# Kernel tuning notes

Measured on AMD Instinct MI355X. Metric: run time of the kernel, lower is better.

The kernel has to match this reference:

```python
import jax, jax.numpy as jnp
import numpy as np

DIM = 384
NH = 12
HEAD = DIM // NH
WS = (7, 7, 7)
L = WS[0] * WS[1] * WS[2]          # 343 tokens per window
NW = 64                             # number of windows (mask.shape[0])
B = 1                               # batch per window group
N = B * NW                          # leading dim of x
TBL = (2 * WS[0] - 1) * (2 * WS[1] - 1) * (2 * WS[2] - 1)  # 2197
SCALE = HEAD ** -0.5


def _rel_index():
    # Standard Swin 3D relative position index, shape (L, L), values in [0, TBL)
    coords = np.stack(np.meshgrid(*[np.arange(w) for w in WS], indexing='ij')).reshape(3, -1)  # (3, L)
    rel = coords[:, :, None] - coords[:, None, :]                     # (3, L, L)
    rel = rel + (np.array(WS) - 1)[:, None, None]                     # shift to >= 0
    s1 = (2 * WS[1] - 1) * (2 * WS[2] - 1)
    s2 = (2 * WS[2] - 1)
    idx = rel[0] * s1 + rel[1] * s2 + rel[2]
    return jnp.asarray(idx, jnp.int32)


def setup_inputs() -> dict:
    key = jax.random.key(0)
    k_x, k_m, k_qkv, k_tbl, k_pw = jax.random.split(key, 5)
    x = jax.random.normal(k_x, (N, L, DIM), dtype=jnp.float32)
    mask = jax.random.bernoulli(k_m, 0.5, (NW, L, L))                 # bool, True = masked
    qkv_w = jax.random.normal(k_qkv, (DIM, 3 * DIM), dtype=jnp.float32) * 0.02
    table = jax.random.normal(k_tbl, (TBL, NH), dtype=jnp.float32) * 0.02
    proj_w = jax.random.normal(k_pw, (DIM, DIM), dtype=jnp.float32) * 0.02
    proj_b = jnp.zeros((DIM,), dtype=jnp.float32)
    rel_idx = _rel_index()
    return {"x": x, "qkv_w": qkv_w, "table": table, "proj_w": proj_w,
            "proj_b": proj_b, "mask": mask, "rel_idx": rel_idx}


def reference(x, qkv_w, table, proj_w, proj_b, mask, rel_idx):
    n, l, _ = x.shape
    # QKV projection (no bias, qkv_bias=False)
    qkv = (x @ qkv_w).reshape(n, l, 3, NH, HEAD).transpose(2, 0, 3, 1, 4)  # (3, n, nh, l, ch)
    q, k, v = qkv[0], qkv[1], qkv[2]
    attn = jnp.einsum('nhlc,nhmc->nhlm', q * SCALE, k)                 # (n, nh, l, l)
    # gather relative position bias: (L*L, nh) -> (nh, L, L)
    bias = table[rel_idx.reshape(-1)].reshape(l, l, NH).transpose(2, 0, 1)
    attn = attn + bias[None]
    # per-window boolean mask: attn viewed as (batch, nw, nh, l, l)
    attn = attn.reshape(-1, NW, NH, l, l)
    attn = jnp.where(mask[None, :, None], -jnp.inf, attn).reshape(n, NH, l, l)
    attn = jax.nn.softmax(attn, axis=-1)
    out = jnp.einsum('nhlm,nhmc->nhlc', attn, v)                       # (n, nh, l, ch)
    out = out.transpose(0, 2, 1, 3).reshape(n, l, DIM)
    return out @ proj_w + proj_b
```

## Files before the change

### kernel.cpp

```cpp
#include <hip/hip_runtime.h>


#define DIMD 384
#define NHH 12
#define HEADD 32
#define LL 343
#define NWW 64
#define NTOK (NWW * LL)
#define MPT 176
#define MP (MPT * 128)
#define LP 352
#define QT 22
#define KS 40
#define VTS 360
#define PSB 40
#define MW 12
#define SCALE_ 0.17677669529663687f
#define LOG2E_ 1.4426950408889634f
#define NEGBIG_ (-1.0e4f)

typedef _Float16 f16;
typedef _Float16 v8h __attribute__((ext_vector_type(8)));
typedef _Float16 v4h __attribute__((ext_vector_type(4)));
typedef float v4f __attribute__((ext_vector_type(4)));

__device__ __forceinline__ void async_cp16(const void* g, void* l) {
    __builtin_amdgcn_global_load_lds(
        (const __attribute__((address_space(1))) void*)g,
        (__attribute__((address_space(3))) void*)l, 16, 0, 0);
}

constexpr size_t QKV_ELEMS = (size_t)NWW * NHH * LL * HEADD;
constexpr size_t OFF_Q    = 0;
constexpr size_t OFF_K    = OFF_Q  + QKV_ELEMS * 2;
constexpr size_t OFF_V    = OFF_K  + QKV_ELEMS * 2;
constexpr size_t OFF_AO   = OFF_V  + QKV_ELEMS * 2;
constexpr size_t OFF_BT   = OFF_AO + (size_t)MP * DIMD * 2;
constexpr size_t OFF_WT   = OFF_BT + (size_t)NHH * LP * LP * 4;
constexpr size_t OFF_PWT  = OFF_WT + (size_t)3 * DIMD * DIMD * 2;
constexpr size_t OFF_MTB  = OFF_PWT + (size_t)DIMD * DIMD * 2;

constexpr int SMEM_ATTN = LP * KS * 2 + 32 * VTS * 2 + LP * MW * 4 + 8 * 16 * PSB * 2;

#define S0 (NTOK * DIMD / 4)
#define S1 (3 * DIMD * DIMD)
#define S2 (DIMD * DIMD)
#define S3 (NHH * LP * LP)
#define S4 (NWW * MW * LP)
#define SPREP (S0 + S1 + S2 + S3 + S4)

__global__ __launch_bounds__(256) void prep_all(
    const float* __restrict__ x, f16* __restrict__ xh,
    const float* __restrict__ qkv_w, f16* __restrict__ wt,
    const float* __restrict__ proj_w, f16* __restrict__ pwt,
    const float* __restrict__ table, const int* __restrict__ rel, float* __restrict__ btf,
    const int* __restrict__ mask, unsigned int* __restrict__ mtb) {
    int t = blockIdx.x * 256 + threadIdx.x;
    if (t < S0) {
        float4 v = *(const float4*)(x + (size_t)t * 4);
        v4h o; o[0] = (f16)v.x; o[1] = (f16)v.y; o[2] = (f16)v.z; o[3] = (f16)v.w;
        *(v4h*)(xh + (size_t)t * 4) = o;
    } else if (t < S0 + S1) {
        int e = t - S0;
        int n = e / DIMD, k = e % DIMD;
        wt[e] = (f16)qkv_w[(size_t)k * (3 * DIMD) + n];
    } else if (t < S0 + S1 + S2) {
        int e = t - S0 - S1;
        int n = e / DIMD, k = e % DIMD;
        pwt[e] = (f16)proj_w[(size_t)k * DIMD + n];
    } else if (t < S0 + S1 + S2 + S3) {
        int e = t - S0 - S1 - S2;
        int h = e / (LP * LP), rem = e % (LP * LP);
        int rq = rem / (LP * 4);
        int rem2 = rem % (LP * 4);
        int col = rem2 >> 2, e2 = rem2 & 3;
        int r = rq * 4 + e2;
        float v = NEGBIG_;
        if (col < LL && r < LL) v = table[(size_t)rel[r * LL + col] * NHH + h] * LOG2E_;
        btf[e] = v;
    } else if (t < SPREP) {
        int e = t - S0 - S1 - S2 - S3;
        int n = e / (MW * LP), rem = e % (MW * LP);
        int wg = rem / LP, col = rem % LP;
        unsigned int wd = 0;
        if (col < LL) {
            int rbase = wg * 32;
#pragma unroll 4
            for (int b = 0; b < 32; ++b) {
                int r = rbase + b;
                if (r < LL && mask[((size_t)n * LL + r) * LL + col]) wd |= (1u << b);
            }
        }
        mtb[((size_t)n * LP + col) * MW + wg] = wd;
    }
}

__global__ __launch_bounds__(256) void qkv_gemm(
    const f16* __restrict__ xh, const f16* __restrict__ wt,
    f16* __restrict__ qb, f16* __restrict__ kb, f16* __restrict__ vb) {
    __shared__ f16 As[128 * 32];
    __shared__ f16 Bs[128 * 32];
    const int lin = blockIdx.x;
    const int m0 = ((lin / 72) * 8 + (lin & 7)) * 128;
    const int n0 = ((lin >> 3) % 9) * 128;
    const int tid = threadIdx.x;
    const int wave = tid >> 6, lane = tid & 63;
    const int quad = lane >> 4, l15 = lane & 15;
    const int wm = (wave >> 1) * 64, wn = (wave & 1) * 64;
    const int srow = (lane >> 2);
    const int scol = (lane & 3) * 8;
    const f16* ga0 = xh + (size_t)(m0 + wave * 32 + srow) * DIMD + scol;
    const f16* ga1 = xh + (size_t)(m0 + wave * 32 + 16 + srow) * DIMD + scol;
    const f16* gb0 = wt + (size_t)(n0 + wave * 32 + srow) * DIMD + scol;
    const f16* gb1 = wt + (size_t)(n0 + wave * 32 + 16 + srow) * DIMD + scol;
    f16* la0 = As + (wave * 2) * 512;
    f16* la1 = As + (wave * 2 + 1) * 512;
    f16* lb0 = Bs + (wave * 2) * 512;
    f16* lb1 = Bs + (wave * 2 + 1) * 512;
    v4f acc[4][4] = {};
    for (int k0 = 0; k0 < DIMD; k0 += 32) {
        async_cp16(ga0 + k0, la0);
        async_cp16(ga1 + k0, la1);
        async_cp16(gb0 + k0, lb0);
        async_cp16(gb1 + k0, lb1);
        __syncthreads();
        v8h a[4], b[4];
#pragma unroll
        for (int i = 0; i < 4; ++i) a[i] = *(const v8h*)(As + (wm + i * 16 + l15) * 32 + quad * 8);
#pragma unroll
        for (int j = 0; j < 4; ++j) b[j] = *(const v8h*)(Bs + (wn + j * 16 + l15) * 32 + quad * 8);
#pragma unroll
        for (int i = 0; i < 4; ++i)
#pragma unroll
            for (int j = 0; j < 4; ++j)
                acc[i][j] = __builtin_amdgcn_mfma_f32_16x16x32_f16(a[i], b[j], acc[i][j], 0, 0, 0);
        __syncthreads();
    }
#pragma unroll
    for (int i = 0; i < 4; ++i)
#pragma unroll
        for (int e = 0; e < 4; ++e) {
            int gm = m0 + wm + i * 16 + quad * 4 + e;
            if (gm < NTOK) {
                int win = gm / LL, tok = gm % LL;
#pragma unroll
                for (int j = 0; j < 4; ++j) {
                    int gn = n0 + wn + j * 16 + l15;
                    int t = gn / DIMD, rem = gn % DIMD;
                    int h = rem >> 5, ch = rem & 31;
                    f16* dst = (t == 0) ? qb : (t == 1) ? kb : vb;
                    float ov = acc[i][j][e];
                    if (t == 0) ov *= (SCALE_ * LOG2E_);
                    dst[(((size_t)(win * NHH + h)) * LL + tok) * HEADD + ch] = (f16)ov;
                }
            }
        }
}

__global__ __launch_bounds__(512, 4) void attn_kernel(
    const f16* __restrict__ qb, const f16* __restrict__ kb, const f16* __restrict__ vb,
    const float* __restrict__ biasT, const unsigned int* __restrict__ mtb,
    f16* __restrict__ ao) {
    extern __shared__ char smem[];
    f16* Ks  = (f16*)smem;
    f16* Vts = Ks + LP * KS;
    unsigned int* mtbL = (unsigned int*)(Vts + 32 * VTS);
    f16* Ps  = (f16*)(mtbL + LP * MW);
    const int n = blockIdx.x, h = blockIdx.y;
    const int tid = threadIdx.x, wave = tid >> 6, lane = tid & 63;
    const int quad = lane >> 4, l15 = lane & 15;
    const size_t slice = ((size_t)(n * NHH + h)) * (LL * HEADD);
    const f16* qg = qb + slice;
    const f16* kg = kb + slice;
    const f16* vg = vb + slice;
    for (int i = tid; i < LL * 8; i += 512) {
        int row = i >> 3, c4 = i & 7;
        *(ushort4*)(Ks + row * KS + c4 * 4) = *(const ushort4*)(kg + i * 4);
    }
    for (int i = tid; i < (LP - LL) * 8; i += 512) {
        int row = LL + (i >> 3), c4 = i & 7;
        *(ushort4*)(Ks + row * KS + c4 * 4) = make_ushort4(0, 0, 0, 0);
    }
    for (int i = tid; i < LL * 8; i += 512) {
        int key = i >> 3, c4 = (i & 7) * 4;
        ushort4 vv = *(const ushort4*)(vg + key * HEADD + c4);
        f16* d = Vts + c4 * VTS + key;
        d[0] = *(const f16*)&vv.x; d[VTS] = *(const f16*)&vv.y;
        d[2 * VTS] = *(const f16*)&vv.z; d[3 * VTS] = *(const f16*)&vv.w;
    }
    for (int i = tid; i < 32 * (LP - LL); i += 512) {
        int ch = i / (LP - LL), key = LL + i % (LP - LL);
        Vts[ch * VTS + key] = (f16)0.f;
    }
    {
        const unsigned int* mg = mtb + (size_t)n * LP * MW;
        for (int i = tid; i < LP * MW; i += 512) mtbL[i] = mg[i];
    }
    __syncthreads();
    f16* Pw = Ps + wave * (16 * PSB);
    const float* bth = biasT + (size_t)h * LP * LP;
    for (int qt = wave; qt < QT; qt += 8) {
        v8h af = *(const v8h*)(qg + (qt * 16 + l15) * HEADD + quad * 8);
        const int r0 = qt * 16 + quad * 4;
        const int rword = r0 >> 5, rsh = r0 & 31;
        const float* bq = bth + (size_t)(qt * 4 + quad) * (LP * 4);
        v4f rsum = {};
        v4f o0 = {}, o1 = {};
#pragma unroll
        for (int ktp = 0; ktp < 11; ++ktp) {
            v4f cin[2]; unsigned int mw[2]; v8h bf[2]; v4f s[2];
#pragma unroll
            for (int half = 0; half < 2; ++half) {
                const int col = (ktp * 2 + half) * 16 + l15;
                cin[half] = *(const v4f*)(bq + (size_t)col * 4);
                mw[half] = mtbL[col * MW + rword];
                bf[half] = *(const v8h*)(Ks + col * KS + quad * 8);
            }
#pragma unroll
            for (int half = 0; half < 2; ++half) {
                v4f c = cin[half];
#pragma unroll
                for (int e = 0; e < 4; ++e)
                    if ((mw[half] >> (rsh + e)) & 1u) c[e] = NEGBIG_;
                s[half] = __builtin_amdgcn_mfma_f32_16x16x32_f16(af, bf[half], c, 0, 0, 0);
            }
#pragma unroll
            for (int half = 0; half < 2; ++half)
#pragma unroll
                for (int e = 0; e < 4; ++e) {
                    float p = __builtin_amdgcn_exp2f(s[half][e]);
                    rsum[e] += p;
                    Pw[(quad * 4 + e) * PSB + half * 16 + l15] = (f16)p;
                }
            v8h a  = *(const v8h*)(Pw + l15 * PSB + quad * 8);
            v8h b0 = *(const v8h*)(Vts + l15 * VTS + ktp * 32 + quad * 8);
            v8h b1 = *(const v8h*)(Vts + (16 + l15) * VTS + ktp * 32 + quad * 8);
            o0 = __builtin_amdgcn_mfma_f32_16x16x32_f16(a, b0, o0, 0, 0, 0);
            o1 = __builtin_amdgcn_mfma_f32_16x16x32_f16(a, b1, o1, 0, 0, 0);
        }
#pragma unroll
        for (int e = 0; e < 4; ++e) {
            float t = rsum[e];
            t += __shfl_xor(t, 1);
            t += __shfl_xor(t, 2);
            t += __shfl_xor(t, 4);
            t += __shfl_xor(t, 8);
            rsum[e] = t;
        }
#pragma unroll
        for (int e = 0; e < 4; ++e) {
            int r = r0 + e;
            if (r < LL) {
                float inv = 1.f / rsum[e];
                f16* orow = ao + ((size_t)(n * LL + r)) * DIMD + h * HEADD;
                orow[l15] = (f16)(o0[e] * inv);
                orow[16 + l15] = (f16)(o1[e] * inv);
            }
        }
    }
}

__global__ __launch_bounds__(256) void proj_gemm(
    const f16* __restrict__ ao, const f16* __restrict__ pwt,
    const float* __restrict__ pb, float* __restrict__ out) {
    __shared__ f16 As[128 * 32];
    __shared__ f16 Bs[128 * 32];
    const int lin = blockIdx.x;
    const int m0 = ((lin / 24) * 8 + (lin & 7)) * 128;
    const int n0 = ((lin >> 3) % 3) * 128;
    const int tid = threadIdx.x;
    const int wave = tid >> 6, lane = tid & 63;
    const int quad = lane >> 4, l15 = lane & 15;
    const int wm = (wave >> 1) * 64, wn = (wave & 1) * 64;
    const int srow = (lane >> 2);
    const int scol = (lane & 3) * 8;
    const f16* ga0 = ao + (size_t)(m0 + wave * 32 + srow) * DIMD + scol;
    const f16* ga1 = ao + (size_t)(m0 + wave * 32 + 16 + srow) * DIMD + scol;
    const f16* gb0 = pwt + (size_t)(n0 + wave * 32 + srow) * DIMD + scol;
    const f16* gb1 = pwt + (size_t)(n0 + wave * 32 + 16 + srow) * DIMD + scol;
    f16* la0 = As + (wave * 2) * 512;
    f16* la1 = As + (wave * 2 + 1) * 512;
    f16* lb0 = Bs + (wave * 2) * 512;
    f16* lb1 = Bs + (wave * 2 + 1) * 512;
    v4f acc[4][4] = {};
    for (int k0 = 0; k0 < DIMD; k0 += 32) {
        async_cp16(ga0 + k0, la0);
        async_cp16(ga1 + k0, la1);
        async_cp16(gb0 + k0, lb0);
        async_cp16(gb1 + k0, lb1);
        __syncthreads();
        v8h a[4], b[4];
#pragma unroll
        for (int i = 0; i < 4; ++i) a[i] = *(const v8h*)(As + (wm + i * 16 + l15) * 32 + quad * 8);
#pragma unroll
        for (int j = 0; j < 4; ++j) b[j] = *(const v8h*)(Bs + (wn + j * 16 + l15) * 32 + quad * 8);
#pragma unroll
        for (int i = 0; i < 4; ++i)
#pragma unroll
            for (int j = 0; j < 4; ++j)
                acc[i][j] = __builtin_amdgcn_mfma_f32_16x16x32_f16(a[i], b[j], acc[i][j], 0, 0, 0);
        __syncthreads();
    }
#pragma unroll
    for (int i = 0; i < 4; ++i)
#pragma unroll
        for (int e = 0; e < 4; ++e) {
            int gm = m0 + wm + i * 16 + quad * 4 + e;
            if (gm < NTOK) {
#pragma unroll
                for (int j = 0; j < 4; ++j) {
                    int gn = n0 + wn + j * 16 + l15;
                    out[(size_t)gm * DIMD + gn] = acc[i][j][e] + pb[gn];
                }
            }
        }
}

extern "C" void kernel_launch(void* const* d_in, const int* in_sizes, int n_in,
                              void* d_out, int out_size, void* d_ws, size_t ws_size,
                              hipStream_t stream) {
    const float* x      = (const float*)d_in[0];
    const float* qkv_w  = (const float*)d_in[1];
    const float* table  = (const float*)d_in[2];
    const float* proj_w = (const float*)d_in[3];
    const float* proj_b = (const float*)d_in[4];
    const int* mask     = (const int*)d_in[5];
    const int* rel      = (const int*)d_in[6];
    float* out = (float*)d_out;
    char* ws = (char*)d_ws;

    f16* q    = (f16*)(ws + OFF_Q);
    f16* k    = (f16*)(ws + OFF_K);
    f16* v    = (f16*)(ws + OFF_V);
    f16* xh   = (f16*)(ws + OFF_AO);
    f16* ao   = (f16*)(ws + OFF_AO);
    float* bt = (float*)(ws + OFF_BT);
    f16* wt   = (f16*)(ws + OFF_WT);
    f16* pwt  = (f16*)(ws + OFF_PWT);
    unsigned int* mtb = (unsigned int*)(ws + OFF_MTB);

    hipFuncSetAttribute((const void*)attn_kernel,
                        hipFuncAttributeMaxDynamicSharedMemorySize, SMEM_ATTN);

    prep_all<<<(SPREP + 255) / 256, 256, 0, stream>>>(
        x, xh, qkv_w, wt, proj_w, pwt, table, rel, bt, mask, mtb);
    qkv_gemm<<<dim3(MPT * 9), 256, 0, stream>>>(xh, wt, q, k, v);
    attn_kernel<<<dim3(NWW, NHH), 512, SMEM_ATTN, stream>>>(q, k, v, bt, mtb, ao);
    proj_gemm<<<dim3(MPT * 3), 256, 0, stream>>>(ao, pwt, proj_b, out);
}
```

Before: 237.9 us.

## Fuse x fp32-to-fp16 conversion into QKV GEMM and use head-major QKV layout

Drops the separate x-to-fp16 conversion pass from the prep kernel. The QKV GEMM now loads fp32 x directly, converts it in registers and writes it to LDS, which saves one full write and read of the fp16 copy of x. The Q/K/V buffers change to a [head][token][ch] layout so the epilogue can use precomputed per-column offsets instead of per-element div/mod. The trade-off is that A-tile loads become synchronous fp32 loads rather than async LDS copies, and each x tile is re-read and re-converted by all 9 N-tiles.

```diff
diff --git a/kernel.cpp b/kernel.cpp
--- a/kernel.cpp
+++ b/kernel.cpp
@@ -30,11 +30,11 @@
         (__attribute__((address_space(3))) void*)l, 16, 0, 0);
 }
 
-constexpr size_t QKV_ELEMS = (size_t)NWW * NHH * LL * HEADD;
+constexpr size_t HBUF = (size_t)NHH * MP * HEADD * 2;
 constexpr size_t OFF_Q    = 0;
-constexpr size_t OFF_K    = OFF_Q  + QKV_ELEMS * 2;
-constexpr size_t OFF_V    = OFF_K  + QKV_ELEMS * 2;
-constexpr size_t OFF_AO   = OFF_V  + QKV_ELEMS * 2;
+constexpr size_t OFF_K    = OFF_Q  + HBUF;
+constexpr size_t OFF_V    = OFF_K  + HBUF;
+constexpr size_t OFF_AO   = OFF_V  + HBUF;
 constexpr size_t OFF_BT   = OFF_AO + (size_t)MP * DIMD * 2;
 constexpr size_t OFF_WT   = OFF_BT + (size_t)NHH * LP * LP * 4;
 constexpr size_t OFF_PWT  = OFF_WT + (size_t)3 * DIMD * DIMD * 2;
@@ -42,34 +42,28 @@
 
 constexpr int SMEM_ATTN = LP * KS * 2 + 32 * VTS * 2 + LP * MW * 4 + 8 * 16 * PSB * 2;
 
-#define S0 (NTOK * DIMD / 4)
 #define S1 (3 * DIMD * DIMD)
 #define S2 (DIMD * DIMD)
 #define S3 (NHH * LP * LP)
 #define S4 (NWW * MW * LP)
-#define SPREP (S0 + S1 + S2 + S3 + S4)
+#define SPREP (S1 + S2 + S3 + S4)
 
 __global__ __launch_bounds__(256) void prep_all(
-    const float* __restrict__ x, f16* __restrict__ xh,
     const float* __restrict__ qkv_w, f16* __restrict__ wt,
     const float* __restrict__ proj_w, f16* __restrict__ pwt,
     const float* __restrict__ table, const int* __restrict__ rel, float* __restrict__ btf,
     const int* __restrict__ mask, unsigned int* __restrict__ mtb) {
     int t = blockIdx.x * 256 + threadIdx.x;
-    if (t < S0) {
-        float4 v = *(const float4*)(x + (size_t)t * 4);
-        v4h o; o[0] = (f16)v.x; o[1] = (f16)v.y; o[2] = (f16)v.z; o[3] = (f16)v.w;
-        *(v4h*)(xh + (size_t)t * 4) = o;
-    } else if (t < S0 + S1) {
-        int e = t - S0;
+    if (t < S1) {
+        int e = t;
         int n = e / DIMD, k = e % DIMD;
         wt[e] = (f16)qkv_w[(size_t)k * (3 * DIMD) + n];
-    } else if (t < S0 + S1 + S2) {
-        int e = t - S0 - S1;
+    } else if (t < S1 + S2) {
+        int e = t - S1;
         int n = e / DIMD, k = e % DIMD;
         pwt[e] = (f16)proj_w[(size_t)k * DIMD + n];
-    } else if (t < S0 + S1 + S2 + S3) {
-        int e = t - S0 - S1 - S2;
+    } else if (t < S1 + S2 + S3) {
+        int e = t - S1 - S2;
         int h = e / (LP * LP), rem = e % (LP * LP);
         int rq = rem / (LP * 4);
         int rem2 = rem % (LP * 4);
@@ -79,7 +73,7 @@
         if (col < LL && r < LL) v = table[(size_t)rel[r * LL + col] * NHH + h] * LOG2E_;
         btf[e] = v;
     } else if (t < SPREP) {
-        int e = t - S0 - S1 - S2 - S3;
+        int e = t - S1 - S2 - S3;
         int n = e / (MW * LP), rem = e % (MW * LP);
         int wg = rem / LP, col = rem % LP;
         unsigned int wd = 0;
@@ -96,7 +90,7 @@
 }
 
 __global__ __launch_bounds__(256) void qkv_gemm(
-    const f16* __restrict__ xh, const f16* __restrict__ wt,
+    const float* __restrict__ x, const f16* __restrict__ wt,
     f16* __restrict__ qb, f16* __restrict__ kb, f16* __restrict__ vb) {
     __shared__ f16 As[128 * 32];
     __shared__ f16 Bs[128 * 32];
@@ -109,20 +103,29 @@
     const int wm = (wave >> 1) * 64, wn = (wave & 1) * 64;
     const int srow = (lane >> 2);
     const int scol = (lane & 3) * 8;
-    const f16* ga0 = xh + (size_t)(m0 + wave * 32 + srow) * DIMD + scol;
-    const f16* ga1 = xh + (size_t)(m0 + wave * 32 + 16 + srow) * DIMD + scol;
     const f16* gb0 = wt + (size_t)(n0 + wave * 32 + srow) * DIMD + scol;
     const f16* gb1 = wt + (size_t)(n0 + wave * 32 + 16 + srow) * DIMD + scol;
-    f16* la0 = As + (wave * 2) * 512;
-    f16* la1 = As + (wave * 2 + 1) * 512;
     f16* lb0 = Bs + (wave * 2) * 512;
     f16* lb1 = Bs + (wave * 2 + 1) * 512;
+    int arow[4]; const float* asrc[4];
+#pragma unroll
+    for (int i = 0; i < 4; ++i) {
+        int c = i * 256 + tid;
+        arow[i] = c >> 3;
+        int srcr = m0 + arow[i]; if (srcr >= NTOK) srcr = NTOK - 1;
+        asrc[i] = x + (size_t)srcr * DIMD + (c & 7) * 4;
+    }
     v4f acc[4][4] = {};
     for (int k0 = 0; k0 < DIMD; k0 += 32) {
-        async_cp16(ga0 + k0, la0);
-        async_cp16(ga1 + k0, la1);
         async_cp16(gb0 + k0, lb0);
         async_cp16(gb1 + k0, lb1);
+#pragma unroll
+        for (int i = 0; i < 4; ++i) {
+            int c = i * 256 + tid;
+            float4 v = *(const float4*)(asrc[i] + k0);
+            v4h o; o[0] = (f16)v.x; o[1] = (f16)v.y; o[2] = (f16)v.z; o[3] = (f16)v.w;
+            *(v4h*)(As + arow[i] * 32 + (c & 7) * 4) = o;
+        }
         __syncthreads();
         v8h a[4], b[4];
 #pragma unroll
@@ -136,23 +139,25 @@
                 acc[i][j] = __builtin_amdgcn_mfma_f32_16x16x32_f16(a[i], b[j], acc[i][j], 0, 0, 0);
         __syncthreads();
     }
+    const int t = n0 / DIMD;
+    f16* dst = (t == 0) ? qb : (t == 1) ? kb : vb;
+    const float sc = (t == 0) ? (SCALE_ * LOG2E_) : 1.0f;
+    size_t hoff[4];
+#pragma unroll
+    for (int j = 0; j < 4; ++j) {
+        int rem = (n0 - t * DIMD) + wn + j * 16 + l15;
+        hoff[j] = (size_t)(rem >> 5) * ((size_t)MP * HEADD) + (rem & 31);
+    }
 #pragma unroll
     for (int i = 0; i < 4; ++i)
 #pragma unroll
         for (int e = 0; e < 4; ++e) {
             int gm = m0 + wm + i * 16 + quad * 4 + e;
             if (gm < NTOK) {
-                int win = gm / LL, tok = gm % LL;
-#pragma unroll
-                for (int j = 0; j < 4; ++j) {
-                    int gn = n0 + wn + j * 16 + l15;
-                    int t = gn / DIMD, rem = gn % DIMD;
-                    int h = rem >> 5, ch = rem & 31;
-                    f16* dst = (t == 0) ? qb : (t == 1) ? kb : vb;
-                    float ov = acc[i][j][e];
-                    if (t == 0) ov *= (SCALE_ * LOG2E_);
-                    dst[(((size_t)(win * NHH + h)) * LL + tok) * HEADD + ch] = (f16)ov;
-                }
+                size_t g32 = (size_t)gm * HEADD;
+#pragma unroll
+                for (int j = 0; j < 4; ++j)
+                    dst[hoff[j] + g32] = (f16)(acc[i][j][e] * sc);
             }
         }
 }
@@ -169,7 +174,7 @@
     const int n = blockIdx.x, h = blockIdx.y;
     const int tid = threadIdx.x, wave = tid >> 6, lane = tid & 63;
     const int quad = lane >> 4, l15 = lane & 15;
-    const size_t slice = ((size_t)(n * NHH + h)) * (LL * HEADD);
+    const size_t slice = ((size_t)h * MP + n * LL) * HEADD;
     const f16* qg = qb + slice;
     const f16* kg = kb + slice;
     const f16* vg = vb + slice;
@@ -332,7 +337,6 @@
     f16* q    = (f16*)(ws + OFF_Q);
     f16* k    = (f16*)(ws + OFF_K);
     f16* v    = (f16*)(ws + OFF_V);
-    f16* xh   = (f16*)(ws + OFF_AO);
     f16* ao   = (f16*)(ws + OFF_AO);
     float* bt = (float*)(ws + OFF_BT);
     f16* wt   = (f16*)(ws + OFF_WT);
@@ -343,8 +347,8 @@
                         hipFuncAttributeMaxDynamicSharedMemorySize, SMEM_ATTN);
 
     prep_all<<<(SPREP + 255) / 256, 256, 0, stream>>>(
-        x, xh, qkv_w, wt, proj_w, pwt, table, rel, bt, mask, mtb);
-    qkv_gemm<<<dim3(MPT * 9), 256, 0, stream>>>(xh, wt, q, k, v);
+        qkv_w, wt, proj_w, pwt, table, rel, bt, mask, mtb);
+    qkv_gemm<<<dim3(MPT * 9), 256, 0, stream>>>(x, wt, q, k, v);
     attn_kernel<<<dim3(NWW, NHH), 512, SMEM_ATTN, stream>>>(q, k, v, bt, mtb, ao);
     proj_gemm<<<dim3(MPT * 3), 256, 0, stream>>>(ao, pwt, proj_b, out);
 }
```

Measured after the change: 240.6 us. No clear change (+1.2%).
